# Performance work log

Hardware: AMD Instinct MI355X
Metric: run time of the kernel (lower is better)

The kernel has to match this reference:

```python
import jax, jax.numpy as jnp
import numpy as np

B, S, DIM, HEADS, HEAD_DIM = 2, 1536, 1024, 16, 64
BLOCK_SIZE, LOOK_AHEAD, LOOK_BACKWARD = 24, 1, 1
ROPE_THETA = 10000.0


def setup_inputs() -> dict:
    key = jax.random.key(0)
    ks = jax.random.split(key, 6)
    s = 0.02  # init scale for weights
    return {
        "x": jax.random.normal(ks[0], (B, S, DIM), jnp.float32),
        "Wq": jax.random.normal(ks[1], (DIM, DIM), jnp.float32) * s,
        "bq": jnp.zeros((DIM,), jnp.float32),
        "Wk": jax.random.normal(ks[2], (DIM, DIM), jnp.float32) * s,
        "bk": jnp.zeros((DIM,), jnp.float32),
        "Wv": jax.random.normal(ks[3], (DIM, DIM), jnp.float32) * s,
        "bv": jnp.zeros((DIM,), jnp.float32),
        "Wo": jax.random.normal(ks[4], (DIM, DIM), jnp.float32) * s,
        "bo": jnp.zeros((DIM,), jnp.float32),
        "position_ids": jnp.arange(S, dtype=jnp.int32),
    }


def _rotate_half(v):
    # pairs (x1, x2) -> (-x2, x1), interleaved (matches torch reshape/unbind/stack)
    v2 = v.reshape(*v.shape[:-1], -1, 2)
    x1, x2 = v2[..., 0], v2[..., 1]
    return jnp.stack((-x2, x1), axis=-1).reshape(v.shape)


def _rope_tables(position_ids):
    # DitRotary: theta_i = 1/ROPE_THETA^(2i/rotary_dim), i=0..31; cos/sin duplicated
    # pairwise -> [c0,c0,c1,c1,...] of length HEAD_DIM
    inv_freq = 1.0 / (ROPE_THETA ** (jnp.arange(0, HEAD_DIM, 2, dtype=jnp.float32) / HEAD_DIM))
    ang = position_ids.astype(jnp.float32)[:, None] * inv_freq[None, :]  # [S, 32]
    cos = jnp.repeat(jnp.cos(ang), 2, axis=-1)  # [S, HEAD_DIM]
    sin = jnp.repeat(jnp.sin(ang), 2, axis=-1)
    return cos, sin


def reference(x, Wq, bq, Wk, bk, Wv, bv, Wo, bo, position_ids):
    b, s, _ = x.shape
    q = (x @ Wq + bq).reshape(b, s, HEADS, HEAD_DIM)
    k = (x @ Wk + bk).reshape(b, s, HEADS, HEAD_DIM)
    v = (x @ Wv + bv).reshape(b, s, HEADS, HEAD_DIM)

    # Partial rotary: applied ONLY to head 0 (torch slices dim=2 == heads)
    cos, sin = _rope_tables(position_ids)            # [S, HEAD_DIM]
    q0 = q[:, :, 0, :] * cos + _rotate_half(q[:, :, 0, :]) * sin
    k0 = k[:, :, 0, :] * cos + _rotate_half(k[:, :, 0, :]) * sin
    q = jnp.concatenate([q0[:, :, None, :], q[:, :, 1:, :]], axis=2)
    k = jnp.concatenate([k0[:, :, None, :], k[:, :, 1:, :]], axis=2)

    # Block-banded mask: diff[i, j] = block(j) - block(i)
    blk = position_ids // BLOCK_SIZE
    diff = blk[None, :] - blk[:, None]               # [S, S]
    allowed = (diff >= -LOOK_BACKWARD) & (diff <= LOOK_AHEAD)
    neg = jnp.where(allowed, 0.0, jnp.finfo(jnp.float32).min)  # ~mask * finfo.min

    scale = 1.0 / jnp.sqrt(jnp.float32(HEAD_DIM))
    scores = jnp.einsum("bqhd,bkhd->bhqk", q, k) * scale + neg[None, None]
    attn = jax.nn.softmax(scores.astype(jnp.float32), axis=-1).astype(q.dtype)
    out = jnp.einsum("bhqk,bkhd->bqhd", attn, v).reshape(b, s, HEADS * HEAD_DIM)
    return out @ Wo + bo
```

## Files before the change

kernel.cpp:

```cpp
#include <hip/hip_runtime.h>
#include <hip/hip_bf16.h>
#include <stdint.h>

typedef _Float16 f16;
typedef _Float16 f16x8 __attribute__((ext_vector_type(8)));
typedef float    f32x4 __attribute__((ext_vector_type(4)));
typedef unsigned short u16;
typedef unsigned int   u32;

#define S_LEN 1536
#define NDIM  1024
#define MROWS 3072

__device__ __forceinline__ u16 f2h(float f){
  _Float16 h = (_Float16)f;
  return __builtin_bit_cast(u16, h);
}

#define GLDS16(g, l) __builtin_amdgcn_global_load_lds( \
    (const __attribute__((address_space(1))) u32*)(const void*)(g), \
    (__attribute__((address_space(3))) u32*)(void*)(l), 16, 0, 0)

__global__ __launch_bounds__(256) void cast_f32_f16(
    const float* __restrict__ in, u16* __restrict__ out)
{
  const int i = blockIdx.x * 256 + threadIdx.x;
  const float4* p = (const float4*)in;
  float4 a = p[i*2], b = p[i*2+1];
  alignas(16) u16 tmp[8];
  tmp[0]=f2h(a.x); tmp[1]=f2h(a.y); tmp[2]=f2h(a.z); tmp[3]=f2h(a.w);
  tmp[4]=f2h(b.x); tmp[5]=f2h(b.y); tmp[6]=f2h(b.z); tmp[7]=f2h(b.w);
  *(uint4*)(out + (size_t)i*8) = *(const uint4*)tmp;
}

__global__ __launch_bounds__(256) void transpose4(
    const float* __restrict__ w0, const float* __restrict__ w1,
    const float* __restrict__ w2, const float* __restrict__ w3,
    u16* __restrict__ out)
{
  const float* W = (blockIdx.z==0)?w0:(blockIdx.z==1)?w1:(blockIdx.z==2)?w2:w3;
  u16* O = out + (size_t)blockIdx.z * (1024u*1024u);
  __shared__ __align__(16) u16 T[64*72];
  const int t = threadIdx.x;
  const int r0 = blockIdx.y*64, c0 = blockIdx.x*64;
  #pragma unroll
  for (int i=0;i<2;i++){
    int v = t + i*256;
    int row = v >> 3, col = (v & 7) * 8;
    const float* src = W + (size_t)(r0+row)*NDIM + c0 + col;
    float4 a = *(const float4*)src;
    float4 b = *(const float4*)(src + 4);
    alignas(16) u16 tmp[8];
    tmp[0]=f2h(a.x); tmp[1]=f2h(a.y); tmp[2]=f2h(a.z); tmp[3]=f2h(a.w);
    tmp[4]=f2h(b.x); tmp[5]=f2h(b.y); tmp[6]=f2h(b.z); tmp[7]=f2h(b.w);
    *(uint4*)(T + row*72 + col) = *(const uint4*)tmp;
  }
  __syncthreads();
  #pragma unroll
  for (int i=0;i<2;i++){
    int v = t + i*256;
    int cc = v >> 3, rr = (v & 7) * 8;
    alignas(16) u16 tmp[8];
    #pragma unroll
    for (int j=0;j<8;j++) tmp[j] = T[(rr+j)*72 + cc];
    *(uint4*)(O + (size_t)(c0+cc)*NDIM + r0 + rr) = *(const uint4*)tmp;
  }
}

#define SUBK 32

template<int TM>
__global__ __launch_bounds__(256) void gemm_bias_rope(
    const u16* __restrict__ A,
    const u16* __restrict__ BT,
    const float* __restrict__ b0, const float* __restrict__ b1,
    const float* __restrict__ b2,
    u16*   __restrict__ Ch,
    float* __restrict__ Cf,
    const int* __restrict__ pos,
    int M, int rope_mats, int f32_out)
{
  constexpr int TN   = 64;
  constexpr int MI   = TM / 32;
  constexpr int AW   = TM / 4;
  constexpr int ABUF = TM * 64;
  constexpr int BBUF = TN * 64;

  __shared__ __align__(16) u16 As[2*ABUF];
  __shared__ __align__(16) u16 Bs[2*BBUF];

  const int t    = threadIdx.x;
  const int lane = t & 63;
  const int wave = t >> 6;
  const int z    = blockIdx.z;
  const int m0   = blockIdx.y * TM;
  const int n0   = blockIdx.x * 64;
  const u16* Bm  = BT + (size_t)z * (1024u*1024u);
  u16*       Cm  = Ch ? (Ch + (size_t)z * ((size_t)M * NDIM)) : (u16*)0;
  const float* bias = (z==0) ? b0 : ((z==1) ? b1 : b2);

  const int wm   = (wave >> 1) * (TM/2);
  const int wn   = (wave & 1) * 32;
  const int l15  = lane & 15;
  const int quad = lane >> 4;

  const int lrow = lane >> 2;
  const int lcol = (lane & 3) * 8;
  const u16* gA = A  + (size_t)(m0 + wave*AW + lrow)*NDIM + lcol;
  const u16* gB = Bm + (size_t)(n0 + wave*16 + lrow)*NDIM + lcol;

  f32x4 acc[MI][2];
  #pragma unroll
  for (int i=0;i<MI;i++)
    #pragma unroll
    for (int j=0;j<2;j++)
      acc[i][j] = (f32x4){0.f,0.f,0.f,0.f};

  auto stage = [&](int k0, int buf) {
    u16* la = As + buf*ABUF + (wave*AW)*SUBK;
    u16* lb = Bs + buf*BBUF + (wave*16)*SUBK;
    #pragma unroll
    for (int kb=0;kb<2;kb++){
      const u16* ga = gA + k0 + kb*SUBK;
      u16* lak = la + kb*(TM*SUBK);
      GLDS16(ga, lak);
      if (TM == 128) GLDS16(ga + 16*NDIM, lak + 16*SUBK);
      GLDS16(gB + k0 + kb*SUBK, lb + kb*(TN*SUBK));
    }
  };
  auto compute = [&](int buf) {
    #pragma unroll
    for (int kb=0;kb<2;kb++){
      f16x8 af[MI], bfr[2];
      #pragma unroll
      for (int i=0;i<MI;i++)
        af[i]  = *(const f16x8*)(As + buf*ABUF + kb*(TM*SUBK)
                                 + (wm + i*16 + l15)*SUBK + quad*8);
      #pragma unroll
      for (int j=0;j<2;j++)
        bfr[j] = *(const f16x8*)(Bs + buf*BBUF + kb*(TN*SUBK)
                                 + (wn + j*16 + l15)*SUBK + quad*8);
      #pragma unroll
      for (int i=0;i<MI;i++)
        #pragma unroll
        for (int j=0;j<2;j++)
          acc[i][j] = __builtin_amdgcn_mfma_f32_16x16x32_f16(
                          af[i], bfr[j], acc[i][j], 0, 0, 0);
    }
  };

  stage(0, 0);
  for (int it = 0; it < 16; it += 2) {
    __syncthreads();
    if (it + 1 < 16) stage((it+1)*64, 1);
    compute(0);
    __syncthreads();
    if (it + 2 < 16) stage((it+2)*64, 0);
    compute(1);
  }

  const bool rope_tile = (z < rope_mats) && (n0 == 0);
  #pragma unroll
  for (int i=0;i<MI;i++){
    const int rbase = m0 + wm + i*16 + quad*4;
    #pragma unroll
    for (int j=0;j<2;j++){
      const int c  = n0 + wn + j*16 + l15;
      const float bv = bias[c];
      f32x4 v4 = acc[i][j];
      #pragma unroll
      for (int r=0;r<4;r++) v4[r] += bv;
      if (rope_tile) {
        const int   ii  = c >> 1;
        const float inv = powf(10000.0f, -(float)ii * (1.0f/32.0f));
        const float sgn = (c & 1) ? 1.0f : -1.0f;
        #pragma unroll
        for (int r=0;r<4;r++){
          float val     = v4[r];
          float partner = __shfl_xor(val, 1, 64);
          int   srow    = (rbase + r) % S_LEN;
          float ang     = (float)pos[srow] * inv;
          float sv, cv;
          sincosf(ang, &sv, &cv);
          v4[r] = val * cv + sgn * partner * sv;
        }
      }
      if (f32_out) {
        #pragma unroll
        for (int r=0;r<4;r++)
          Cf[(size_t)(rbase + r)*NDIM + c] = v4[r];
      } else {
        #pragma unroll
        for (int r=0;r<4;r++)
          Cm[(size_t)(rbase + r)*NDIM + c] = f2h(v4[r]);
      }
    }
  }
}

__global__ __launch_bounds__(256) void attn_kernel(
    const u16* __restrict__ q, const u16* __restrict__ k,
    const u16* __restrict__ v, u16* __restrict__ o)
{
  const int qb = blockIdx.x;
  const int h  = blockIdx.y;
  const int b  = blockIdx.z;
  const int t  = threadIdx.x;
  const int lane = t & 63;
  const int wave = t >> 6;
  const int l15  = lane & 15;
  const int quad = lane >> 4;

  const int ks_ = (qb == 0) ? 0 : (qb - 1) * 24;
  const int ke_ = min(S_LEN, (qb + 2) * 24);
  const int kn  = ke_ - ks_;

  __shared__ __align__(16) u16   Qs[32*72];
  __shared__ __align__(16) u16   Ks[80*72];
  __shared__ __align__(16) u16   Vt[64*104];
  __shared__ __align__(16) float Ss[32*80];
  __shared__ __align__(16) u16   Ps[32*104];

  const size_t qrow0 = (size_t)b*S_LEN + qb*24;
  const size_t krow0 = (size_t)b*S_LEN + ks_;
  const int hoff = h * 64;

  if (t < 192) {
    int row = t >> 3, col = (t & 7) * 8;
    *(uint4*)(Qs + row*72 + col) = *(const uint4*)(q + (qrow0+row)*NDIM + hoff + col);
  }
  for (int e = t; e < kn*8; e += 256) {
    int row = e >> 3, col = (e & 7) * 8;
    *(uint4*)(Ks + row*72 + col) = *(const uint4*)(k + (krow0+row)*NDIM + hoff + col);
    uint4 vv = *(const uint4*)(v + (krow0+row)*NDIM + hoff + col);
    const u16* pu = (const u16*)&vv;
    #pragma unroll
    for (int j=0;j<8;j++) Vt[(col+j)*104 + row] = pu[j];
  }
  for (int e = t; e < 64*48; e += 256) {
    int d = e / 48, c = 48 + (e - (e/48)*48);
    if (c >= kn) Vt[d*104 + c] = 0;
  }
  __syncthreads();

  const int ntn = (kn + 15) >> 4;
  for (int id = wave; id < 2*ntn; id += 4) {
    int mt = id / ntn, nt = id - (id/ntn)*ntn;
    f32x4 acc = (f32x4){0.f,0.f,0.f,0.f};
    #pragma unroll
    for (int ks2 = 0; ks2 < 2; ks2++) {
      f16x8 a = *(const f16x8*)(Qs + (mt*16 + l15)*72 + ks2*32 + quad*8);
      f16x8 bb= *(const f16x8*)(Ks + (nt*16 + l15)*72 + ks2*32 + quad*8);
      acc = __builtin_amdgcn_mfma_f32_16x16x32_f16(a, bb, acc, 0, 0, 0);
    }
    #pragma unroll
    for (int r=0;r<4;r++)
      Ss[(mt*16 + quad*4 + r)*80 + nt*16 + l15] = acc[r] * 0.125f;
  }
  __syncthreads();

  #pragma unroll
  for (int i=0;i<6;i++){
    int row = wave*6 + i;
    float v0 = (lane      < kn) ? Ss[row*80 + lane]      : -1e30f;
    float v1 = (lane + 64 < kn) ? Ss[row*80 + 64 + lane] : -1e30f;
    float m = fmaxf(v0, v1);
    #pragma unroll
    for (int off=32; off; off>>=1) m = fmaxf(m, __shfl_xor(m, off, 64));
    float p0 = __expf(v0 - m);
    float p1 = __expf(v1 - m);
    float s = p0 + p1;
    #pragma unroll
    for (int off=32; off; off>>=1) s += __shfl_xor(s, off, 64);
    float inv = 1.0f / s;
    Ps[row*104 + lane] = f2h(p0 * inv);
    if (lane < 32) Ps[row*104 + 64 + lane] = f2h(p1 * inv);
  }
  __syncthreads();

  const int kceil = (kn + 31) >> 5;
  #pragma unroll
  for (int id2 = 0; id2 < 2; id2++){
    int id = wave*2 + id2;
    int mt = id >> 2, nt = id & 3;
    f32x4 acc = (f32x4){0.f,0.f,0.f,0.f};
    for (int ks2 = 0; ks2 < kceil; ks2++) {
      f16x8 a = *(const f16x8*)(Ps + (mt*16 + l15)*104 + ks2*32 + quad*8);
      f16x8 bb= *(const f16x8*)(Vt + (nt*16 + l15)*104 + ks2*32 + quad*8);
      acc = __builtin_amdgcn_mfma_f32_16x16x32_f16(a, bb, acc, 0, 0, 0);
    }
    #pragma unroll
    for (int r=0;r<4;r++){
      int row = mt*16 + quad*4 + r;
      if (row < 24)
        o[(qrow0 + row)*NDIM + hoff + nt*16 + l15] = f2h(acc[r]);
    }
  }
}

extern "C" void kernel_launch(void* const* d_in, const int* in_sizes, int n_in,
                              void* d_out, int out_size, void* d_ws, size_t ws_size,
                              hipStream_t stream)
{
  const float* x   = (const float*)d_in[0];
  const float* Wq  = (const float*)d_in[1];
  const float* bq  = (const float*)d_in[2];
  const float* Wk  = (const float*)d_in[3];
  const float* bk  = (const float*)d_in[4];
  const float* Wv  = (const float*)d_in[5];
  const float* bv  = (const float*)d_in[6];
  const float* Wo  = (const float*)d_in[7];
  const float* bo  = (const float*)d_in[8];
  const int*   pos = (const int*)d_in[9];

  u16* ws   = (u16*)d_ws;
  u16* WT   = ws;
  u16* xb   = WT + 4u*1024u*1024u;
  u16* qkv  = xb + (size_t)MROWS*NDIM;
  u16* attn = WT;
  float* outf = (float*)d_out;

  cast_f32_f16<<<dim3(MROWS*NDIM/(256*8)), 256, 0, stream>>>(x, xb);
  transpose4<<<dim3(16,16,4), 256, 0, stream>>>(Wq, Wk, Wv, Wo, WT);
  gemm_bias_rope<128><<<dim3(16,24,3), 256, 0, stream>>>(
      xb, WT, bq, bk, bv, qkv, nullptr, pos, MROWS, 2, 0);
  attn_kernel<<<dim3(64,16,2), 256, 0, stream>>>(
      qkv, qkv + (size_t)MROWS*NDIM, qkv + 2u*(size_t)MROWS*NDIM, attn);
  gemm_bias_rope<64><<<dim3(16,48,1), 256, 0, stream>>>(
      attn, WT + 3u*1024u*1024u, bo, bo, bo, nullptr, outf, pos, MROWS,
      0, 1);
}
```

Baseline: 185.7 us.

## Replace double-buffered LDS pipeline with single-buffered GEMM main loop

The GEMM main loop drops its two-stage LDS double buffering and switches to a single buffer: each k-step loads a tile, synchronizes, computes, then synchronizes again. This halves shared memory use, which may allow more resident blocks per CU. In exchange, global-to-LDS loads no longer overlap with MFMA compute within a block, so the loop relies on other waves to hide memory latency.

Result: faster. 176.7 us (-4.9%).

```diff
diff --git a/kernel.cpp b/kernel.cpp
--- a/kernel.cpp
+++ b/kernel.cpp
@@ -83,11 +83,9 @@
   constexpr int TN   = 64;
   constexpr int MI   = TM / 32;
   constexpr int AW   = TM / 4;
-  constexpr int ABUF = TM * 64;
-  constexpr int BBUF = TN * 64;
-
-  __shared__ __align__(16) u16 As[2*ABUF];
-  __shared__ __align__(16) u16 Bs[2*BBUF];
+
+  __shared__ __align__(16) u16 As[TM*64];
+  __shared__ __align__(16) u16 Bs[TN*64];
 
   const int t    = threadIdx.x;
   const int lane = t & 63;
@@ -108,6 +106,8 @@
   const int lcol = (lane & 3) * 8;
   const u16* gA = A  + (size_t)(m0 + wave*AW + lrow)*NDIM + lcol;
   const u16* gB = Bm + (size_t)(n0 + wave*16 + lrow)*NDIM + lcol;
+  u16* lA = As + (wave*AW)*SUBK;
+  u16* lB = Bs + (wave*16)*SUBK;
 
   f32x4 acc[MI][2];
   #pragma unroll
@@ -116,30 +116,25 @@
     for (int j=0;j<2;j++)
       acc[i][j] = (f32x4){0.f,0.f,0.f,0.f};
 
-  auto stage = [&](int k0, int buf) {
-    u16* la = As + buf*ABUF + (wave*AW)*SUBK;
-    u16* lb = Bs + buf*BBUF + (wave*16)*SUBK;
+  for (int k0 = 0; k0 < 1024; k0 += 64) {
     #pragma unroll
     for (int kb=0;kb<2;kb++){
       const u16* ga = gA + k0 + kb*SUBK;
-      u16* lak = la + kb*(TM*SUBK);
+      u16* lak = lA + kb*(TM*SUBK);
       GLDS16(ga, lak);
       if (TM == 128) GLDS16(ga + 16*NDIM, lak + 16*SUBK);
-      GLDS16(gB + k0 + kb*SUBK, lb + kb*(TN*SUBK));
-    }
-  };
-  auto compute = [&](int buf) {
+      GLDS16(gB + k0 + kb*SUBK, lB + kb*(TN*SUBK));
+    }
+    __syncthreads();
     #pragma unroll
     for (int kb=0;kb<2;kb++){
       f16x8 af[MI], bfr[2];
       #pragma unroll
       for (int i=0;i<MI;i++)
-        af[i]  = *(const f16x8*)(As + buf*ABUF + kb*(TM*SUBK)
-                                 + (wm + i*16 + l15)*SUBK + quad*8);
+        af[i]  = *(const f16x8*)(As + kb*(TM*SUBK) + (wm + i*16 + l15)*SUBK + quad*8);
       #pragma unroll
       for (int j=0;j<2;j++)
-        bfr[j] = *(const f16x8*)(Bs + buf*BBUF + kb*(TN*SUBK)
-                                 + (wn + j*16 + l15)*SUBK + quad*8);
+        bfr[j] = *(const f16x8*)(Bs + kb*(TN*SUBK) + (wn + j*16 + l15)*SUBK + quad*8);
       #pragma unroll
       for (int i=0;i<MI;i++)
         #pragma unroll
@@ -147,16 +142,7 @@
           acc[i][j] = __builtin_amdgcn_mfma_f32_16x16x32_f16(
                           af[i], bfr[j], acc[i][j], 0, 0, 0);
     }
-  };
-
-  stage(0, 0);
-  for (int it = 0; it < 16; it += 2) {
     __syncthreads();
-    if (it + 1 < 16) stage((it+1)*64, 1);
-    compute(0);
-    __syncthreads();
-    if (it + 2 < 16) stage((it+2)*64, 0);
-    compute(1);
   }
 
   const bool rope_tile = (z < rope_mats) && (n0 == 0);
```
